# Optimization experiments

Measured on AMD Instinct MI355X. Metric: run time of the kernel, lower is better.

The kernel has to match this reference:

```python
import jax, jax.numpy as jnp
import numpy as np


def setup_inputs() -> dict:
    key = jax.random.key(0)
    k0, k1, k2, k3 = jax.random.split(key, 4)
    B, C_IN, H, W = 8, 256, 64, 64
    O, NUM = 256, 8  # output channels, number of regions
    mat0 = jax.random.normal(k0, (B, C_IN, H, W), dtype=jnp.float32)
    mat1 = jax.random.normal(k1, (O, C_IN, NUM), dtype=jnp.float32)  # per-region 1x1 filters (shared across batch, batch_W=1)
    mask = jax.random.uniform(k2, (NUM, H, W), dtype=jnp.float32)    # soft region weights per pixel
    Alpha = jax.random.uniform(k3, (NUM,), dtype=jnp.float32)        # per-region modulation scale
    return {"mat0": mat0, "mat1": mat1, "mask": mask, "Alpha": Alpha, "use_alpha": 1, "beta": 1}


def reference(mat0, mat1, mask, Alpha, use_alpha, beta):
    # Deformable (region-aware) matmul: for each pixel (h,w), apply the
    # region-r filter mat1[:, :, r] to mat0[:, :, h, w], weighted by the
    # per-pixel soft region mask (optionally alpha-modulated per region).
    # out[b,o,h,w] = sum_r sum_c mat0[b,c,h,w] * mat1[o,c,r] * Alpha[r] * mask[r,h,w]
    m1 = mat1 * Alpha if use_alpha else mat1  # [O, C, R] scaled per region
    return jnp.einsum('bchw,ocr,rhw->bohw', mat0, m1, mask)
```

## Files before the change

kernel.cpp:

```cpp
#include <hip/hip_runtime.h>
#include <hip/hip_bf16.h>
#include <stdint.h>


typedef __attribute__((ext_vector_type(8)))  short short8;
typedef __attribute__((ext_vector_type(16))) float f32x16;

#define C_IN  256
#define HW_   4096
#define NRND  32

__device__ __forceinline__ short f2bf(float x) {
  union { __hip_bfloat16 h; short s; } u;
  u.h = __float2bfloat16(x);
  return u.s;
}

__global__ __launch_bounds__(256) void prep_w_kernel(
    const float* __restrict__ mat1, const float* __restrict__ Alpha,
    const int* __restrict__ use_alpha, short* __restrict__ Aprep) {
  int t = blockIdx.x * 256 + threadIdx.x;
  int o = t & 255;
  int c = t >> 8;
  int ua = use_alpha[0];
  const float* src = mat1 + ((size_t)o * C_IN + c) * 8;
  short8 v;
#pragma unroll
  for (int r = 0; r < 8; ++r) {
    float s = ua ? Alpha[r] : 1.0f;
    v[r] = f2bf(src[r] * s);
  }
  *(short8*)(Aprep + ((size_t)c * 256 + o) * 8) = v;
}

__global__ __launch_bounds__(256, 2) void gemm_deform_kernel(
    const float* __restrict__ mat0, const short* __restrict__ Aprep,
    const float* __restrict__ mask, float* __restrict__ out) {
  __shared__ short8 A_lds[2][1024];

  int bid = blockIdx.x;
  int wg = (bid & 7) * 64 + (bid >> 3);
  int tile_m = wg & 1;
  int tile_n = wg >> 1;
  int o0 = tile_m * 128;
  int n0 = tile_n * 128;
  int b  = n0 >> 12;
  int p0 = n0 & 4095;

  int t    = threadIdx.x;
  int lane = t & 63;
  int w    = t >> 6;
  int wc   = w & 1;
  int wr   = w >> 1;
  int l31  = lane & 31;
  int cr   = lane >> 5;

  int colb = p0 + wc * 64 + l31;
  float mk[2][8];
#pragma unroll
  for (int ni = 0; ni < 2; ++ni)
#pragma unroll
    for (int r = 0; r < 8; ++r)
      mk[ni][r] = mask[r * HW_ + colb + ni * 32];

  const float* __restrict__ m0b =
      mat0 + ((size_t)b * C_IN + cr) * HW_ + colb;

  const __attribute__((address_space(1))) uint32_t* gA =
      (const __attribute__((address_space(1))) uint32_t*)Aprep;
  int soo  = (w & 1) * 64 + lane;
  int scqb = w >> 1;

  f32x16 acc[2][2];
#pragma unroll
  for (int mi = 0; mi < 2; ++mi)
#pragma unroll
    for (int ni = 0; ni < 2; ++ni)
#pragma unroll
      for (int j = 0; j < 16; ++j) acc[mi][ni][j] = 0.f;

  float P0[4][2], P1[4][2];

  auto STAGE = [&](int rd, int buf) {
    __attribute__((address_space(3))) uint32_t* lA =
        (__attribute__((address_space(3))) uint32_t*)&A_lds[buf][0];
#pragma unroll
    for (int i = 0; i < 4; ++i) {
      int gslot = (rd * 8 + i * 2 + scqb) * 256 + o0 + soo;
      __builtin_amdgcn_global_load_lds(gA + (size_t)gslot * 4,
                                       lA + (size_t)(i * 256 + w * 64) * 4,
                                       16, 0, 0);
    }
  };

  auto LOADP = [&](float (&P)[4][2], int rd) {
    const float* mp = m0b + (size_t)(rd * 8) * HW_;
#pragma unroll
    for (int kq = 0; kq < 4; ++kq) {
      P[kq][0] = mp[(size_t)(kq * 2) * HW_];
      P[kq][1] = mp[(size_t)(kq * 2) * HW_ + 32];
    }
  };

  auto COMP = [&](const short8* __restrict__ Abuf, float (&P)[4][2], int rd) {
    int rp = rd + 2 > 31 ? 31 : rd + 2;
    const float* mnext = m0b + (size_t)(rp * 8) * HW_;
#pragma unroll
    for (int kq = 0; kq < 4; ++kq) {
      short8 a0 = Abuf[(kq * 2 + cr) * 128 + wr * 64 + l31];
      short8 a1 = Abuf[(kq * 2 + cr) * 128 + wr * 64 + 32 + l31];
      short8 bv0, bv1;
#pragma unroll
      for (int r = 0; r < 8; ++r) {
        bv0[r] = f2bf(P[kq][0] * mk[0][r]);
        bv1[r] = f2bf(P[kq][1] * mk[1][r]);
      }
      acc[0][0] = __builtin_amdgcn_mfma_f32_32x32x16_bf16(a0, bv0, acc[0][0], 0, 0, 0);
      acc[0][1] = __builtin_amdgcn_mfma_f32_32x32x16_bf16(a0, bv1, acc[0][1], 0, 0, 0);
      acc[1][0] = __builtin_amdgcn_mfma_f32_32x32x16_bf16(a1, bv0, acc[1][0], 0, 0, 0);
      acc[1][1] = __builtin_amdgcn_mfma_f32_32x32x16_bf16(a1, bv1, acc[1][1], 0, 0, 0);
      P[kq][0] = mnext[(size_t)(kq * 2) * HW_];
      P[kq][1] = mnext[(size_t)(kq * 2) * HW_ + 32];
    }
  };

  STAGE(0, 0);
  LOADP(P0, 0);
  LOADP(P1, 1);
  __syncthreads();

#pragma unroll 1
  for (int rd = 0; rd < NRND; rd += 2) {
    STAGE(rd + 1, 1);
    COMP(&A_lds[0][0], P0, rd);
    __syncthreads();
    if (rd + 2 < NRND) STAGE(rd + 2, 0);
    COMP(&A_lds[1][0], P1, rd + 1);
    __syncthreads();
  }

  size_t obase = (size_t)b * 256 * HW_ + colb;
#pragma unroll
  for (int mi = 0; mi < 2; ++mi) {
#pragma unroll
    for (int ni = 0; ni < 2; ++ni) {
#pragma unroll
      for (int reg = 0; reg < 16; ++reg) {
        int row = o0 + wr * 64 + mi * 32 + (reg & 3) + 8 * (reg >> 2) + 4 * cr;
        out[obase + (size_t)row * HW_ + ni * 32] = acc[mi][ni][reg];
      }
    }
  }
}

extern "C" void kernel_launch(void* const* d_in, const int* in_sizes, int n_in,
                              void* d_out, int out_size, void* d_ws, size_t ws_size,
                              hipStream_t stream) {
  const float* mat0      = (const float*)d_in[0];
  const float* mat1      = (const float*)d_in[1];
  const float* mask      = (const float*)d_in[2];
  const float* Alpha     = (const float*)d_in[3];
  const int*   use_alpha = (const int*)d_in[4];
  (void)in_sizes; (void)n_in; (void)out_size; (void)ws_size;

  short* Aprep = (short*)d_ws;
  float* outp  = (float*)d_out;

  prep_w_kernel<<<256, 256, 0, stream>>>(mat1, Alpha, use_alpha, Aprep);
  gemm_deform_kernel<<<512, 256, 0, stream>>>(mat0, Aprep, mask, outp);
}
```

Baseline: 53.30 us.

## Switch MFMA operands from bf16 to fp16 and relax barrier waitcnts

```diff
diff --git a/kernel.cpp b/kernel.cpp
--- a/kernel.cpp
+++ b/kernel.cpp
@@ -3,40 +3,34 @@
 #include <stdint.h>
 
 
-typedef __attribute__((ext_vector_type(8)))  short short8;
-typedef __attribute__((ext_vector_type(16))) float f32x16;
+typedef __attribute__((ext_vector_type(8)))  _Float16 half8;
+typedef __attribute__((ext_vector_type(16))) float    f32x16;
 
 #define C_IN  256
 #define HW_   4096
 #define NRND  32
 
-__device__ __forceinline__ short f2bf(float x) {
-  union { __hip_bfloat16 h; short s; } u;
-  u.h = __float2bfloat16(x);
-  return u.s;
-}
-
 __global__ __launch_bounds__(256) void prep_w_kernel(
     const float* __restrict__ mat1, const float* __restrict__ Alpha,
-    const int* __restrict__ use_alpha, short* __restrict__ Aprep) {
+    const int* __restrict__ use_alpha, _Float16* __restrict__ Aprep) {
   int t = blockIdx.x * 256 + threadIdx.x;
   int o = t & 255;
   int c = t >> 8;
   int ua = use_alpha[0];
   const float* src = mat1 + ((size_t)o * C_IN + c) * 8;
-  short8 v;
+  half8 v;
 #pragma unroll
   for (int r = 0; r < 8; ++r) {
     float s = ua ? Alpha[r] : 1.0f;
-    v[r] = f2bf(src[r] * s);
+    v[r] = (_Float16)(src[r] * s);
   }
-  *(short8*)(Aprep + ((size_t)c * 256 + o) * 8) = v;
+  *(half8*)(Aprep + ((size_t)c * 256 + o) * 8) = v;
 }
 
 __global__ __launch_bounds__(256, 2) void gemm_deform_kernel(
-    const float* __restrict__ mat0, const short* __restrict__ Aprep,
+    const float* __restrict__ mat0, const _Float16* __restrict__ Aprep,
     const float* __restrict__ mask, float* __restrict__ out) {
-  __shared__ short8 A_lds[2][1024];
+  __shared__ half8 A_lds[2][1024];
 
   int bid = blockIdx.x;
   int wg = (bid & 7) * 64 + (bid >> 3);
@@ -56,12 +50,12 @@
   int cr   = lane >> 5;
 
   int colb = p0 + wc * 64 + l31;
-  float mk[2][8];
+  half8 mkh[2];
 #pragma unroll
   for (int ni = 0; ni < 2; ++ni)
 #pragma unroll
     for (int r = 0; r < 8; ++r)
-      mk[ni][r] = mask[r * HW_ + colb + ni * 32];
+      mkh[ni][r] = (_Float16)mask[r * HW_ + colb + ni * 32];
 
   const float* __restrict__ m0b =
       mat0 + ((size_t)b * C_IN + cr) * HW_ + colb;
@@ -102,23 +96,23 @@
     }
   };
 
-  auto COMP = [&](const short8* __restrict__ Abuf, float (&P)[4][2], int rd) {
+  auto COMP = [&](const half8* __restrict__ Abuf, float (&P)[4][2], int rd) {
     int rp = rd + 2 > 31 ? 31 : rd + 2;
     const float* mnext = m0b + (size_t)(rp * 8) * HW_;
 #pragma unroll
     for (int kq = 0; kq < 4; ++kq) {
-      short8 a0 = Abuf[(kq * 2 + cr) * 128 + wr * 64 + l31];
-      short8 a1 = Abuf[(kq * 2 + cr) * 128 + wr * 64 + 32 + l31];
-      short8 bv0, bv1;
-#pragma unroll
-      for (int r = 0; r < 8; ++r) {
-        bv0[r] = f2bf(P[kq][0] * mk[0][r]);
-        bv1[r] = f2bf(P[kq][1] * mk[1][r]);
-      }
-      acc[0][0] = __builtin_amdgcn_mfma_f32_32x32x16_bf16(a0, bv0, acc[0][0], 0, 0, 0);
-      acc[0][1] = __builtin_amdgcn_mfma_f32_32x32x16_bf16(a0, bv1, acc[0][1], 0, 0, 0);
-      acc[1][0] = __builtin_amdgcn_mfma_f32_32x32x16_bf16(a1, bv0, acc[1][0], 0, 0, 0);
-      acc[1][1] = __builtin_amdgcn_mfma_f32_32x32x16_bf16(a1, bv1, acc[1][1], 0, 0, 0);
+      half8 a0 = Abuf[(kq * 2 + cr) * 128 + wr * 64 + l31];
+      half8 a1 = Abuf[(kq * 2 + cr) * 128 + wr * 64 + 32 + l31];
+      _Float16 h0 = (_Float16)P[kq][0];
+      _Float16 h1 = (_Float16)P[kq][1];
+      half8 pb0 = {h0, h0, h0, h0, h0, h0, h0, h0};
+      half8 pb1 = {h1, h1, h1, h1, h1, h1, h1, h1};
+      half8 bv0 = pb0 * mkh[0];
+      half8 bv1 = pb1 * mkh[1];
+      acc[0][0] = __builtin_amdgcn_mfma_f32_32x32x16_f16(a0, bv0, acc[0][0], 0, 0, 0);
+      acc[0][1] = __builtin_amdgcn_mfma_f32_32x32x16_f16(a0, bv1, acc[0][1], 0, 0, 0);
+      acc[1][0] = __builtin_amdgcn_mfma_f32_32x32x16_f16(a1, bv0, acc[1][0], 0, 0, 0);
+      acc[1][1] = __builtin_amdgcn_mfma_f32_32x32x16_f16(a1, bv1, acc[1][1], 0, 0, 0);
       P[kq][0] = mnext[(size_t)(kq * 2) * HW_];
       P[kq][1] = mnext[(size_t)(kq * 2) * HW_ + 32];
     }
@@ -127,16 +121,19 @@
   STAGE(0, 0);
   LOADP(P0, 0);
   LOADP(P1, 1);
-  __syncthreads();
+  asm volatile("s_waitcnt vmcnt(16)" ::: "memory");
+  __builtin_amdgcn_s_barrier();
 
 #pragma unroll 1
   for (int rd = 0; rd < NRND; rd += 2) {
     STAGE(rd + 1, 1);
     COMP(&A_lds[0][0], P0, rd);
-    __syncthreads();
+    asm volatile("s_waitcnt vmcnt(8)" ::: "memory");
+    __builtin_amdgcn_s_barrier();
     if (rd + 2 < NRND) STAGE(rd + 2, 0);
     COMP(&A_lds[1][0], P1, rd + 1);
-    __syncthreads();
+    asm volatile("s_waitcnt vmcnt(8)" ::: "memory");
+    __builtin_amdgcn_s_barrier();
   }
 
   size_t obase = (size_t)b * 256 * HW_ + colb;
@@ -163,7 +160,7 @@
   const int*   use_alpha = (const int*)d_in[4];
   (void)in_sizes; (void)n_in; (void)out_size; (void)ws_size;
 
-  short* Aprep = (short*)d_ws;
+  _Float16* Aprep = (_Float16*)d_ws;
   float* outp  = (float*)d_out;
 
   prep_w_kernel<<<256, 256, 0, stream>>>(mat1, Alpha, use_alpha, Aprep);
```

Measured after the change: 48.13 us. -9.7%, faster.
